# Optimization experiments

Hardware: AMD Instinct MI355X
Metric: run time of the kernel (lower is better)

## Reference

```python
import jax, jax.numpy as jnp
import numpy as np

G_RATIO = 0.5      # config.g_ratio (enable_train_g_ratio=False)
TMAX = 0.25        # config.Tmax
TB_FACTOR = 0.001


def _expand(x, kernel):
    # x: [B,H,W]; 3x3 neighbor conv, padding 1 (torch F.conv2d with shared filter)
    y = jax.lax.conv_general_dilated(
        x[:, None], kernel, (1, 1), 'SAME',
        dimension_numbers=('NCHW', 'OIHW', 'NCHW'))
    return y[:, 0]


def _st_softmax_noexp(val):
    # straight-through: normalized scores forward -> hard one-hot of argmax
    B = val.shape[0]
    v = val.reshape(B, -1)
    y = v / v.sum(-1, keepdims=True)
    ind = jnp.argmax(y, axis=-1)
    y_hard = jax.nn.one_hot(ind, y.shape[-1], dtype=y.dtype)
    return (jax.lax.stop_gradient(y_hard - y) + y).reshape(val.shape)


def _get_heuristic(goal_maps, tb_factor=TB_FACTOR):
    B, H, W = goal_maps.shape
    loc = jnp.stack(jnp.meshgrid(jnp.arange(H), jnp.arange(W), indexing='ij'), 0)
    loc = loc.astype(goal_maps.dtype)                      # [2,H,W]
    loc_expand = loc.reshape(2, -1)[None]                  # [1,2,HW]
    goal_loc = jnp.einsum('kij,bij->bk', loc, goal_maps)[:, :, None]  # [B,2,1]
    dxdy = jnp.abs(loc_expand - goal_loc)                  # [B,2,HW]
    h = dxdy.sum(1) - dxdy.min(1)                          # chebyshev-ish
    euc = jnp.sqrt(((loc_expand - goal_loc) ** 2).sum(1))
    return (h + tb_factor * euc).reshape(goal_maps.shape)


def _backtrack(goal_maps, parents, num_steps):
    # follow parent pointers from goal, marking path cells
    B = goal_maps.shape[0]
    parents_i = parents.astype(jnp.int32)                  # [B,HW]
    goal_flat = goal_maps.reshape(B, -1).astype(jnp.int32)
    loc = (parents_i * goal_flat).sum(-1)                  # parent of goal
    bidx = jnp.arange(B)

    def body(carry, _):
        path, loc = carry
        valid = loc >= 0
        safe = jnp.where(valid, loc, 0)
        path = path.at[bidx, safe].max(valid.astype(path.dtype))
        loc = jnp.where(valid, parents_i[bidx, safe], loc)
        return (path, loc), None

    (path, _), _ = jax.lax.scan(body, (goal_flat, loc), None, length=num_steps)
    return path.reshape(goal_maps.shape)


def setup_inputs() -> dict:
    key = jax.random.key(0)
    B, H, W = 32, 32, 32
    k1, k2, k3, k4 = jax.random.split(key, 4)
    cost_maps = jax.random.uniform(k1, (B, H, W), dtype=jnp.float32) + 0.1
    si = jax.random.randint(k2, (B,), 0, H * W)
    gi = jax.random.randint(k3, (B,), 0, H * W)
    gi = jnp.where(gi == si, (gi + 1) % (H * W), gi)
    start_maps = jax.nn.one_hot(si, H * W, dtype=jnp.float32).reshape(B, H, W)
    goal_maps = jax.nn.one_hot(gi, H * W, dtype=jnp.float32).reshape(B, H, W)
    obstacles = (jax.random.uniform(k4, (B, H, W)) > 0.1).astype(jnp.float32)
    flat = obstacles.reshape(B, -1)
    flat = flat.at[jnp.arange(B), si].set(1.0).at[jnp.arange(B), gi].set(1.0)
    obstacles_maps = flat.reshape(B, H, W)
    return {'cost_maps': cost_maps, 'start_maps': start_maps,
            'goal_maps': goal_maps, 'obstacles_maps': obstacles_maps}


def reference(cost_maps, start_maps, goal_maps, obstacles_maps):
    B, H, W = cost_maps.shape
    # 8-neighbor filter (num_dirs=8): 3x3 ones with zero center
    kernel = jnp.ones((1, 1, 3, 3), cost_maps.dtype).at[0, 0, 1, 1].set(0.0)
    h = _get_heuristic(goal_maps) + cost_maps
    g0 = jnp.zeros_like(start_maps)
    open0 = start_maps
    hist0 = jnp.zeros_like(start_maps)
    goal_idx = jnp.argmax(goal_maps.reshape(B, -1), -1)
    parents0 = jnp.broadcast_to(
        goal_idx[:, None].astype(cost_maps.dtype), (B, H * W))
    T = int(TMAX * H * W)
    size_norm = np.sqrt(W).astype(np.float32)

    def step(carry, _):
        g, open_maps, histories, parents = carry
        f = G_RATIO * g + (1.0 - G_RATIO) * h
        f_exp = jnp.exp(-f / size_norm) * open_maps
        sel = _st_softmax_noexp(f_exp)                    # [B,H,W]
        dist_to_goal = (sel * goal_maps).sum((1, 2), keepdims=True)
        is_unsolved = (dist_to_goal < 1e-8).astype(g.dtype)
        histories = jnp.clip(histories + sel, 0.0, 1.0)
        open_maps = jnp.clip(open_maps - is_unsolved * sel, 0.0, 1.0)
        neighbor = _expand(sel, kernel) * obstacles_maps
        g2 = _expand((g + cost_maps) * sel, kernel)
        idx = (1.0 - open_maps) * (1.0 - histories) * neighbor
        idx = jnp.clip(idx + open_maps * neighbor * (g2 < g).astype(g.dtype),
                       0.0, 1.0)
        g = jax.lax.stop_gradient(g2 * idx + g * (1.0 - idx))
        open_maps = jax.lax.stop_gradient(jnp.clip(open_maps + idx, 0.0, 1.0))
        idx_f = idx.reshape(B, -1)
        new_parents = jnp.argmax(sel.reshape(B, -1), -1)[:, None]
        new_parents = new_parents.astype(parents.dtype)
        parents = new_parents * idx_f + parents * (1.0 - idx_f)
        return (g, open_maps, histories, parents), None

    (g, open_maps, histories, parents), _ = jax.lax.scan(
        step, (g0, open0, hist0, parents0), None, length=T)
    path_maps = _backtrack(goal_maps, parents, T)
    return histories, path_maps
```

## Files before the change

kernel.cpp:

```cpp
#include <hip/hip_runtime.h>

#define HW 1024
#define TSTEPS 256
#define SIZE_NORM 5.65685424949238019521f

#define REP16(M)  M(0) M(1) M(2) M(3) M(4) M(5) M(6) M(7) M(8) M(9) M(10) M(11) M(12) M(13) M(14) M(15)
#define REP16D(M) M(15) M(14) M(13) M(12) M(11) M(10) M(9) M(8) M(7) M(6) M(5) M(4) M(3) M(2) M(1) M(0)

__device__ __forceinline__ unsigned umax2(unsigned a, unsigned b) { return a > b ? a : b; }
__device__ __forceinline__ unsigned umax3(unsigned a, unsigned b, unsigned c) {
    return umax2(umax2(a, b), c);
}
__device__ __forceinline__ int imin2(int a, int b) { return a < b ? a : b; }

__device__ __forceinline__ float e_of(float g, float h) {
    float f = 0.5f * g + 0.5f * h;
    return expf(-f / SIZE_NORM);
}

#define DPP_MAX(v, ctrl)                                                                     \
    do {                                                                                     \
        unsigned _o = (unsigned)__builtin_amdgcn_mov_dpp((int)(v), (ctrl), 0xF, 0xF, false); \
        (v) = umax2((v), _o);                                                                \
    } while (0)

#define DPP_MIN(v, ctrl)                                                                     \
    do {                                                                                     \
        int _o = __builtin_amdgcn_mov_dpp((v), (ctrl), 0xF, 0xF, false);                     \
        (v) = imin2((v), _o);                                                                \
    } while (0)

__launch_bounds__(64)
__global__ void astar_kernel(const float* __restrict__ cost,
                             const float* __restrict__ start,
                             const float* __restrict__ goal,
                             const float* __restrict__ obst,
                             float* __restrict__ out) {
    __shared__ int   ls_par[HW];
    __shared__ unsigned char ls_m[HW];

    const int b    = blockIdx.x;
    const int lane = threadIdx.x;
    const float* costb  = cost  + b * HW;
    const float* startb = start + b * HW;
    const float* goalb  = goal  + b * HW;
    const float* obstb  = obst  + b * HW;

    const int rowbase = lane >> 5;
    const int col     = lane & 31;

#define DECL_STATE(K) float cst##K, g##K, h##K; unsigned e##K;
    REP16(DECL_STATE)
#undef DECL_STATE
    unsigned openm = 0, histm = 0, obstm = 0, goalm = 0;

#define LOADK(K) { int c = (K)*64 + lane;                                  \
        cst##K = costb[c]; g##K = 0.0f;                                    \
        openm |= (startb[c] > 0.5f ? 1u : 0u) << (K);                      \
        obstm |= (obstb[c]  > 0.5f ? 1u : 0u) << (K);                      \
        goalm |= (goalb[c]  > 0.5f ? 1u : 0u) << (K); }
    REP16(LOADK)
#undef LOADK

    int gidx = 0;
#define GOALK(K) { unsigned long long m = __ballot((goalm >> (K)) & 1u);   \
        if (m) gidx = (K)*64 + (int)(__ffsll(m) - 1); }
    REP16D(GOALK)
#undef GOALK

    const float gi = (float)(gidx >> 5), gj = (float)(gidx & 31);
#define HINITK(K) { int c = (K)*64 + lane;                                 \
        float ci = (float)(c >> 5), cj = (float)(c & 31);                  \
        float dx = fabsf(ci - gi), dy = fabsf(cj - gj);                    \
        float hc = (dx + dy) - fminf(dx, dy);                              \
        float euc = sqrtf(dx * dx + dy * dy);                              \
        float heur = __fadd_rn(hc, __fmul_rn(0.001f, euc));                \
        h##K = __fadd_rn(heur, cst##K);                                    \
        e##K = ((openm >> (K)) & 1u) ? __float_as_uint(e_of(0.0f, h##K)) : 0u; \
        ls_par[c] = gidx; }
    REP16(HINITK)
#undef HINITK

#define UPD(K) {                                                                   \
        const int di_ = (((K) << 1) + rowbase) - si;                               \
        const bool rowok_ = (unsigned)(di_ + 1) <= 2u;                             \
        const bool nb_ = rowok_ && colok && ((di_ != 0) || djnz) &&                \
                         (((obstm >> (K)) & 1u) != 0u);                            \
        const bool op_ = ((openm >> (K)) & 1u) != 0u;                              \
        const bool hs_ = ((histm >> (K)) & 1u) != 0u;                              \
        const bool sel_ = nb_ && ((!op_ && !hs_) || (op_ && (gval < g##K)));       \
        unsigned eN_ = __float_as_uint(e_of(gval, h##K));                          \
        if (sel_) ls_par[(K) * 64 + lane] = s_sel;                                 \
        chg = sel_ ? 1u : chg;                                                     \
        g##K = sel_ ? gval : g##K;                                                 \
        e##K = sel_ ? eN_ : e##K;                                                  \
        openm = sel_ ? (openm | (1u << (K))) : openm;                              \
        {                                                                          \
            const bool isl_ = (k_s == (K)) && (lane == lane_s);                    \
            chg = (isl_ && !hs_) ? 1u : chg;                                       \
            histm = isl_ ? (histm | (1u << (K))) : histm;                          \
            if (unsolved) {                                                        \
                openm = isl_ ? (openm & ~(1u << (K))) : openm;                     \
                e##K  = isl_ ? 0u : e##K;                                          \
            }                                                                      \
        } }

#define CASEU(LBL, CA, CB)                                                            \
    case LBL: {                                                                       \
        const int gb0_ = __builtin_amdgcn_readlane(__float_as_int(g##CA),   lane_s);  \
        const int cb0_ = __builtin_amdgcn_readlane(__float_as_int(cst##CA), lane_s);  \
        const int gb1_ = __builtin_amdgcn_readlane(__float_as_int(g##CB),   lane_s);  \
        const int cb1_ = __builtin_amdgcn_readlane(__float_as_int(cst##CB), lane_s);  \
        const bool hi_ = (k_s != (CA));                                               \
        const float gval = __int_as_float(hi_ ? gb1_ : gb0_) +                        \
                           __int_as_float(hi_ ? cb1_ : cb0_);                         \
        UPD(CA)  UPD(CB)                                                              \
    } break;

    for (int step = 0; step < TSTEPS; ++step) {
        unsigned m0 = umax3(e0,  e1,  e2);
        unsigned m1 = umax3(e3,  e4,  e5);
        unsigned m2 = umax3(e6,  e7,  e8);
        unsigned m3 = umax3(e9,  e10, e11);
        unsigned m4 = umax3(e12, e13, e14);
        unsigned lm = umax2(umax3(m0, m1, m2), umax3(m3, m4, e15));
        DPP_MAX(lm, 0xB1);
        DPP_MAX(lm, 0x4E);
        DPP_MAX(lm, 0x141);
        DPP_MAX(lm, 0x128);
        unsigned r0 = (unsigned)__builtin_amdgcn_readlane((int)lm, 0);
        unsigned r1 = (unsigned)__builtin_amdgcn_readlane((int)lm, 16);
        unsigned r2 = (unsigned)__builtin_amdgcn_readlane((int)lm, 32);
        unsigned r3 = (unsigned)__builtin_amdgcn_readlane((int)lm, 48);
        const unsigned gmax = umax2(umax2(r0, r1), umax2(r2, r3));

#define CD4(Ka, Kb, Kc, Kd, NOUT)                                                  \
        int NOUT; {                                                                \
            int ca_ = (e##Ka == gmax) ? ((Ka) * 64 + lane) : 0x7FFFFFFF;           \
            int cb2_ = (e##Kb == gmax) ? ((Kb) * 64 + lane) : 0x7FFFFFFF;          \
            int cc_ = (e##Kc == gmax) ? ((Kc) * 64 + lane) : 0x7FFFFFFF;           \
            int cd_ = (e##Kd == gmax) ? ((Kd) * 64 + lane) : 0x7FFFFFFF;           \
            NOUT = imin2(imin2(ca_, cb2_), imin2(cc_, cd_));                       \
        }
        CD4(0, 1, 2, 3,    n0_)
        CD4(4, 5, 6, 7,    n1_)
        CD4(8, 9, 10, 11,  n2_)
        CD4(12, 13, 14, 15, n3_)
#undef CD4
        int lmc = imin2(imin2(n0_, n1_), imin2(n2_, n3_));
        DPP_MIN(lmc, 0xB1);
        DPP_MIN(lmc, 0x4E);
        DPP_MIN(lmc, 0x141);
        DPP_MIN(lmc, 0x128);
        int q0 = __builtin_amdgcn_readlane(lmc, 0);
        int q1 = __builtin_amdgcn_readlane(lmc, 16);
        int q2 = __builtin_amdgcn_readlane(lmc, 32);
        int q3 = __builtin_amdgcn_readlane(lmc, 48);
        const int s_sel = imin2(imin2(q0, q1), imin2(q2, q3));

        const int si = s_sel >> 5, sj = s_sel & 31;
        const int lane_s = s_sel & 63, k_s = s_sel >> 6;
        const bool unsolved = (s_sel != gidx);
        const int dj = col - sj;
        const bool colok = (unsigned)(dj + 1) <= 2u;
        const bool djnz = (dj != 0);

        unsigned chg = 0;

        const int k0 = (si > 0 ? si - 1 : 0) >> 1;
        switch (k0) {
            CASEU(0,  0,  1)
            CASEU(1,  1,  2)
            CASEU(2,  2,  3)
            CASEU(3,  3,  4)
            CASEU(4,  4,  5)
            CASEU(5,  5,  6)
            CASEU(6,  6,  7)
            CASEU(7,  7,  8)
            CASEU(8,  8,  9)
            CASEU(9,  9,  10)
            CASEU(10, 10, 11)
            CASEU(11, 11, 12)
            CASEU(12, 12, 13)
            CASEU(13, 13, 14)
            CASEU(14, 14, 15)
            CASEU(15, 14, 15)
            default: break;
        }

        if (!unsolved) {
            if (__ballot(chg != 0u) == 0ull) break;
        }
    }

#define MINITK(K) { int c = (K)*64 + lane; ls_m[c] = (c == gidx) ? 1 : 0; }
    REP16(MINITK)
#undef MINITK
    __syncthreads();
    int A0 = ls_par[gidx];
    if (lane == 0) ls_m[A0] = 1;
    __syncthreads();

    for (int j = 0; j < 8; ++j) {
#define DECLBT(K) int pk##K, pp##K;
        REP16(DECLBT)
#undef DECLBT
        unsigned mk = 0;
#define BT1(K) pk##K = ls_par[(K)*64 + lane];
        REP16(BT1)
#undef BT1
#define BT2(K) pp##K = ls_par[pk##K];
        REP16(BT2)
#undef BT2
#define BT3(K) mk |= (unsigned)ls_m[(K)*64 + lane] << (K);
        REP16(BT3)
#undef BT3
        __syncthreads();
#define BT4(K) if ((mk >> (K)) & 1u) ls_m[pk##K] = 1;
        REP16(BT4)
#undef BT4
#define BT5(K) ls_par[(K)*64 + lane] = pp##K;
        REP16(BT5)
#undef BT5
        __syncthreads();
    }

    float* hout = out + (size_t)b * HW;
    float* pout = out + (size_t)gridDim.x * HW + (size_t)b * HW;
#define OUTK(K) { int c = (K)*64 + lane;                                   \
        hout[c] = (float)((histm >> (K)) & 1u);                            \
        pout[c] = (float)ls_m[c]; }
    REP16(OUTK)
#undef OUTK
}

extern "C" void kernel_launch(void* const* d_in, const int* in_sizes, int n_in,
                              void* d_out, int out_size, void* d_ws, size_t ws_size,
                              hipStream_t stream) {
    (void)n_in; (void)d_ws; (void)ws_size; (void)out_size;
    const float* cost  = (const float*)d_in[0];
    const float* start = (const float*)d_in[1];
    const float* goal  = (const float*)d_in[2];
    const float* obst  = (const float*)d_in[3];
    float* out = (float*)d_out;
    const int nb = in_sizes[0] / HW;
    astar_kernel<<<dim3(nb), dim3(64), 0, stream>>>(cost, start, goal, obst, out);
}
```

Baseline: 40.99 us.

## Fuse argmax and index/g-cost selection into single packed wave reduction

Replaces the two-pass selection (max reduction over scores, then min-index reduction among ties) with a single reduction over a packed (score, reversed index) key that also carries the selected cell's g+cost value. Each cell now caches g+cost, so the per-step readlane of g and cost from the selected lane inside the switch is removed. The wave reduction uses row_shr DPP plus row_bcast steps, reading the result from lane 63. This saves one full reduction chain and several readlanes per step, at the cost of 64-bit compares, three DPP moves per stage and 16 extra registers.

```diff
diff --git a/kernel.cpp b/kernel.cpp
--- a/kernel.cpp
+++ b/kernel.cpp
@@ -7,10 +7,6 @@
 #define REP16(M)  M(0) M(1) M(2) M(3) M(4) M(5) M(6) M(7) M(8) M(9) M(10) M(11) M(12) M(13) M(14) M(15)
 #define REP16D(M) M(15) M(14) M(13) M(12) M(11) M(10) M(9) M(8) M(7) M(6) M(5) M(4) M(3) M(2) M(1) M(0)
 
-__device__ __forceinline__ unsigned umax2(unsigned a, unsigned b) { return a > b ? a : b; }
-__device__ __forceinline__ unsigned umax3(unsigned a, unsigned b, unsigned c) {
-    return umax2(umax2(a, b), c);
-}
 __device__ __forceinline__ int imin2(int a, int b) { return a < b ? a : b; }
 
 __device__ __forceinline__ float e_of(float g, float h) {
@@ -18,17 +14,17 @@
     return expf(-f / SIZE_NORM);
 }
 
-#define DPP_MAX(v, ctrl)                                                                     \
-    do {                                                                                     \
-        unsigned _o = (unsigned)__builtin_amdgcn_mov_dpp((int)(v), (ctrl), 0xF, 0xF, false); \
-        (v) = umax2((v), _o);                                                                \
-    } while (0)
-
-#define DPP_MIN(v, ctrl)                                                                     \
-    do {                                                                                     \
-        int _o = __builtin_amdgcn_mov_dpp((v), (ctrl), 0xF, 0xF, false);                     \
-        (v) = imin2((v), _o);                                                                \
-    } while (0)
+#define PMX(HA, LA, GA, HB, LB, GB) {                                              \
+        unsigned long long a_ = ((unsigned long long)(HA) << 32) | (LA);           \
+        unsigned long long b_ = ((unsigned long long)(HB) << 32) | (LB);           \
+        const bool t_ = b_ > a_;                                                   \
+        HA = t_ ? (HB) : (HA); LA = t_ ? (LB) : (LA); GA = t_ ? (GB) : (GA); }
+
+#define RST(ctrl) {                                                                          \
+        unsigned oh_ = (unsigned)__builtin_amdgcn_mov_dpp((int)ph0, (ctrl), 0xF, 0xF, true); \
+        unsigned ol_ = (unsigned)__builtin_amdgcn_mov_dpp((int)pl0, (ctrl), 0xF, 0xF, true); \
+        int      og_ = __builtin_amdgcn_mov_dpp(pg0, (ctrl), 0xF, 0xF, true);                \
+        PMX(ph0, pl0, pg0, oh_, ol_, og_) }
 
 __launch_bounds__(64)
 __global__ void astar_kernel(const float* __restrict__ cost,
@@ -48,8 +44,9 @@
 
     const int rowbase = lane >> 5;
     const int col     = lane & 31;
-
-#define DECL_STATE(K) float cst##K, g##K, h##K; unsigned e##K;
+    const unsigned nl = 63 - lane;
+
+#define DECL_STATE(K) float cst##K, g##K, h##K, gc##K; unsigned e##K;
     REP16(DECL_STATE)
 #undef DECL_STATE
     unsigned openm = 0, histm = 0, obstm = 0, goalm = 0;
@@ -77,6 +74,7 @@
         float heur = __fadd_rn(hc, __fmul_rn(0.001f, euc));                \
         h##K = __fadd_rn(heur, cst##K);                                    \
         e##K = ((openm >> (K)) & 1u) ? __float_as_uint(e_of(0.0f, h##K)) : 0u; \
+        gc##K = cst##K;                                     \
         ls_par[c] = gidx; }
     REP16(HINITK)
 #undef HINITK
@@ -90,10 +88,12 @@
         const bool hs_ = ((histm >> (K)) & 1u) != 0u;                              \
         const bool sel_ = nb_ && ((!op_ && !hs_) || (op_ && (gval < g##K)));       \
         unsigned eN_ = __float_as_uint(e_of(gval, h##K));                          \
+        float gcN_ = gval + cst##K;                                                \
         if (sel_) ls_par[(K) * 64 + lane] = s_sel;                                 \
         chg = sel_ ? 1u : chg;                                                     \
-        g##K = sel_ ? gval : g##K;                                                 \
-        e##K = sel_ ? eN_ : e##K;                                                  \
+        g##K  = sel_ ? gval : g##K;                                                \
+        gc##K = sel_ ? gcN_ : gc##K;                                               \
+        e##K  = sel_ ? eN_ : e##K;                                                 \
         openm = sel_ ? (openm | (1u << (K))) : openm;                              \
         {                                                                          \
             const bool isl_ = (k_s == (K)) && (lane == lane_s);                    \
@@ -105,58 +105,31 @@
             }                                                                      \
         } }
 
-#define CASEU(LBL, CA, CB)                                                            \
-    case LBL: {                                                                       \
-        const int gb0_ = __builtin_amdgcn_readlane(__float_as_int(g##CA),   lane_s);  \
-        const int cb0_ = __builtin_amdgcn_readlane(__float_as_int(cst##CA), lane_s);  \
-        const int gb1_ = __builtin_amdgcn_readlane(__float_as_int(g##CB),   lane_s);  \
-        const int cb1_ = __builtin_amdgcn_readlane(__float_as_int(cst##CB), lane_s);  \
-        const bool hi_ = (k_s != (CA));                                               \
-        const float gval = __int_as_float(hi_ ? gb1_ : gb0_) +                        \
-                           __int_as_float(hi_ ? cb1_ : cb0_);                         \
-        UPD(CA)  UPD(CB)                                                              \
-    } break;
+#define CASEU(LBL, CA, CB) case LBL: { UPD(CA) UPD(CB) } break;
 
     for (int step = 0; step < TSTEPS; ++step) {
-        unsigned m0 = umax3(e0,  e1,  e2);
-        unsigned m1 = umax3(e3,  e4,  e5);
-        unsigned m2 = umax3(e6,  e7,  e8);
-        unsigned m3 = umax3(e9,  e10, e11);
-        unsigned m4 = umax3(e12, e13, e14);
-        unsigned lm = umax2(umax3(m0, m1, m2), umax3(m3, m4, e15));
-        DPP_MAX(lm, 0xB1);
-        DPP_MAX(lm, 0x4E);
-        DPP_MAX(lm, 0x141);
-        DPP_MAX(lm, 0x128);
-        unsigned r0 = (unsigned)__builtin_amdgcn_readlane((int)lm, 0);
-        unsigned r1 = (unsigned)__builtin_amdgcn_readlane((int)lm, 16);
-        unsigned r2 = (unsigned)__builtin_amdgcn_readlane((int)lm, 32);
-        unsigned r3 = (unsigned)__builtin_amdgcn_readlane((int)lm, 48);
-        const unsigned gmax = umax2(umax2(r0, r1), umax2(r2, r3));
-
-#define CD4(Ka, Kb, Kc, Kd, NOUT)                                                  \
-        int NOUT; {                                                                \
-            int ca_ = (e##Ka == gmax) ? ((Ka) * 64 + lane) : 0x7FFFFFFF;           \
-            int cb2_ = (e##Kb == gmax) ? ((Kb) * 64 + lane) : 0x7FFFFFFF;          \
-            int cc_ = (e##Kc == gmax) ? ((Kc) * 64 + lane) : 0x7FFFFFFF;           \
-            int cd_ = (e##Kd == gmax) ? ((Kd) * 64 + lane) : 0x7FFFFFFF;           \
-            NOUT = imin2(imin2(ca_, cb2_), imin2(cc_, cd_));                       \
-        }
-        CD4(0, 1, 2, 3,    n0_)
-        CD4(4, 5, 6, 7,    n1_)
-        CD4(8, 9, 10, 11,  n2_)
-        CD4(12, 13, 14, 15, n3_)
-#undef CD4
-        int lmc = imin2(imin2(n0_, n1_), imin2(n2_, n3_));
-        DPP_MIN(lmc, 0xB1);
-        DPP_MIN(lmc, 0x4E);
-        DPP_MIN(lmc, 0x141);
-        DPP_MIN(lmc, 0x128);
-        int q0 = __builtin_amdgcn_readlane(lmc, 0);
-        int q1 = __builtin_amdgcn_readlane(lmc, 16);
-        int q2 = __builtin_amdgcn_readlane(lmc, 32);
-        int q3 = __builtin_amdgcn_readlane(lmc, 48);
-        const int s_sel = imin2(imin2(q0, q1), imin2(q2, q3));
+#define PK(K) unsigned ph##K = e##K, pl##K = nl + (15 - (K)) * 64;                 \
+        int pg##K = __float_as_int(gc##K);
+        REP16(PK)
+#undef PK
+#define PM(A, B) PMX(ph##A, pl##A, pg##A, ph##B, pl##B, pg##B)
+        PM(0, 1)   PM(2, 3)   PM(4, 5)   PM(6, 7)
+        PM(8, 9)   PM(10, 11) PM(12, 13) PM(14, 15)
+        PM(0, 2)   PM(4, 6)   PM(8, 10)  PM(12, 14)
+        PM(0, 4)   PM(8, 12)
+        PM(0, 8)
+#undef PM
+        RST(0x111)
+        RST(0x112)
+        RST(0x114)
+        RST(0x118)
+        RST(0x142)
+        RST(0x143)
+
+        const int rl_idx = __builtin_amdgcn_readlane((int)pl0, 63);
+        const int rl_gc  = __builtin_amdgcn_readlane(pg0, 63);
+        const int s_sel  = 1023 - rl_idx;
+        const float gval = __int_as_float(rl_gc);
 
         const int si = s_sel >> 5, sj = s_sel & 31;
         const int lane_s = s_sel & 63, k_s = s_sel >> 6;
```

Result: no change. 40.69 us (-0.7%).
